# Kernel tuning notes

Measured on AMD Instinct MI355X. Metric: run time of the kernel, lower is better.

Reference implementation:

```python
import jax, jax.numpy as jnp
import numpy as np

H = 256          # LSTM hidden size
P = 1            # proj_size
L = 5            # num LSTM layers
T = 1000         # sequence length (forced by Linear(1000, 100))


def _uniform(key, shape, scale):
    return jax.random.uniform(key, shape, dtype=jnp.float32, minval=-scale, maxval=scale)


def setup_inputs() -> dict:
    key = jax.random.key(0)
    ks = jax.random.split(key, 16)
    B = 128
    s = 1.0 / np.sqrt(H)  # PyTorch LSTM init scale
    inp = {
        "x": jax.random.normal(ks[0], (B, T, 1), dtype=jnp.float32),
        # stacked LSTM params: layer input dim is 1 for all layers (input_size=1, proj_size=1)
        "Wih": _uniform(ks[1], (L, 4 * H, 1), s),
        "Whh": _uniform(ks[2], (L, 4 * H, P), s),
        "bih": _uniform(ks[3], (L, 4 * H), s),
        "bhh": _uniform(ks[4], (L, 4 * H), s),
        "Whr": _uniform(ks[5], (L, P, H), s),
        # MLP head
        "W1": _uniform(ks[6], (100, 1000), 1.0 / np.sqrt(1000)),
        "b1": _uniform(ks[7], (100,), 1.0 / np.sqrt(1000)),
        "W2": _uniform(ks[8], (100, 100), 0.1),
        "b2": _uniform(ks[9], (100,), 0.1),
        "W3": _uniform(ks[10], (100, 100), 0.1),
        "b3": _uniform(ks[11], (100,), 0.1),
        "W4": _uniform(ks[12], (1, 100), 0.1),
        "b4": _uniform(ks[13], (1,), 0.1),
    }
    return inp


def _lstm_layer(x_seq, Wih, Whh, bih, bhh, Whr):
    """One projected LSTM layer. x_seq: [B, T, in_dim] -> [B, T, P]."""
    B = x_seq.shape[0]
    # precompute input contribution for all timesteps: [B, T, 4H]
    gx = jnp.einsum('bti,gi->btg', x_seq, Wih) + bih + bhh
    gx = jnp.transpose(gx, (1, 0, 2))  # [T, B, 4H] for scan

    def step(carry, g_t):
        h, c = carry                      # h: [B, P], c: [B, H]
        gates = g_t + h @ Whh.T           # [B, 4H]
        i = jax.nn.sigmoid(gates[:, 0 * H:1 * H])
        f = jax.nn.sigmoid(gates[:, 1 * H:2 * H])
        g = jnp.tanh(gates[:, 2 * H:3 * H])
        o = jax.nn.sigmoid(gates[:, 3 * H:4 * H])
        c = f * c + i * g
        h = (o * jnp.tanh(c)) @ Whr.T     # projected hidden: [B, P]
        return (h, c), h

    h0 = jnp.zeros((B, P), x_seq.dtype)
    c0 = jnp.zeros((B, H), x_seq.dtype)
    _, hs = jax.lax.scan(step, (h0, c0), gx)  # hs: [T, B, P]
    return jnp.transpose(hs, (1, 0, 2))       # [B, T, P]


def reference(x, Wih, Whh, bih, bhh, Whr, W1, b1, W2, b2, W3, b3, W4, b4):
    out = x
    for l in range(L):  # fixed 5 stacked layers
        out = _lstm_layer(out, Wih[l], Whh[l], bih[l], bhh[l], Whr[l])
    out = out[:, :, 0]                      # squeeze -> [B, 1000]
    out = jax.nn.sigmoid(out @ W1.T + b1)   # linear1 + Sigmoid
    out = jax.nn.sigmoid(out @ W2.T + b2)   # linear2 + Sigmoid
    out = jax.nn.relu(out @ W3.T + b3)      # linear3 + ReLU
    out = out @ W4.T + b4                   # linear4 -> [B, 1]
    return out
```

## Files before the change

### kernel.cpp

```cpp
#include <hip/hip_runtime.h>


#define LAYERS 5
#define TT 1000
#define BATCH 128
#define CH 40
#define NCH (TT / CH)

#define LOG2E 1.4426950408889634f

__device__ __forceinline__ float fast_exp2(float x) {
#if __has_builtin(__builtin_amdgcn_exp2f)
  return __builtin_amdgcn_exp2f(x);
#else
  return __exp2f(x);
#endif
}
__device__ __forceinline__ float fast_rcp(float x) {
#if __has_builtin(__builtin_amdgcn_rcpf)
  return __builtin_amdgcn_rcpf(x);
#else
  return 1.0f / x;
#endif
}
__device__ __forceinline__ float fast_sigmoid(float z) {
  float e = fast_exp2(-LOG2E * z);
  return fast_rcp(1.0f + e);
}

template <int CTRL>
__device__ __forceinline__ float dpp_add(float v) {
  int moved = __builtin_amdgcn_update_dpp(0, __builtin_bit_cast(int, v),
                                          CTRL, 0xF, 0xF, false);
  return v + __builtin_bit_cast(float, moved);
}

__device__ __forceinline__ float wave_sum_uniform(float v) {
  v = dpp_add<0x128>(v);
  v = dpp_add<0x124>(v);
  v = dpp_add<0x122>(v);
  v = dpp_add<0x121>(v);
  v = dpp_add<0x142>(v);
  v = dpp_add<0x143>(v);
  return __builtin_bit_cast(float, __builtin_amdgcn_readlane(__builtin_bit_cast(int, v), 63));
}

__device__ __forceinline__ float lane_bcast(float v, int s) {
  return __builtin_bit_cast(float, __builtin_amdgcn_readlane(__builtin_bit_cast(int, v), s));
}

__global__ __launch_bounds__(64, 1) void lstm_wave_kernel(
    const float* __restrict__ x,
    const float* __restrict__ Wih,
    const float* __restrict__ Whh,
    const float* __restrict__ bih,
    const float* __restrict__ bhh,
    const float* __restrict__ Whr,
    float* __restrict__ seq,
    int* __restrict__ flags)
{
  const int bid  = blockIdx.x;
  const int l    = bid >> 7;
  const int b    = bid & 127;
  const int lane = threadIdx.x;

  float wix[4][4], whx[4][4], gb[4][4], whr[4], cc[4];
  const int base = l * 1024;
#pragma unroll
  for (int g = 0; g < 4; ++g) {
    const float sc = (g == 2) ? (-2.0f * LOG2E) : (-LOG2E);
#pragma unroll
    for (int k = 0; k < 4; ++k) {
      int j = base + g * 256 + k * 64 + lane;
      wix[g][k] = Wih[j] * sc;
      whx[g][k] = Whh[j] * sc;
      gb[g][k]  = (bih[j] + bhh[j]) * sc;
    }
  }
#pragma unroll
  for (int k = 0; k < 4; ++k) {
    whr[k] = Whr[l * 256 + k * 64 + lane];
    cc[k] = 0.0f;
  }

  const float* in  = (l == 0) ? (x + b * TT) : (seq + ((l - 1) * BATCH + b) * TT);
  float*       out = seq + (l * BATCH + b) * TT;
  int*       my_flag = flags + l * BATCH + b;
  const int* in_flag = (l > 0) ? (flags + (l - 1) * BATCH + b) : (const int*)flags;

  float h = 0.0f;
  for (int c = 0; c < NCH; ++c) {
    if (l > 0) {
      while (__hip_atomic_load(in_flag, __ATOMIC_ACQUIRE,
                               __HIP_MEMORY_SCOPE_AGENT) <= c)
        __builtin_amdgcn_s_sleep(2);
    }
    float xv = 0.0f;
    if (lane < CH) {
      if (l == 0)
        xv = in[c * CH + lane];
      else
        xv = __hip_atomic_load(in + c * CH + lane, __ATOMIC_RELAXED,
                               __HIP_MEMORY_SCOPE_AGENT);
    }

    float outv = 0.0f;
#pragma unroll 2
    for (int s = 0; s < CH; ++s) {
      const float xs = lane_bcast(xv, s);

      float gx[4][4];
#pragma unroll
      for (int g = 0; g < 4; ++g)
#pragma unroll
        for (int k = 0; k < 4; ++k)
          gx[g][k] = fmaf(xs, wix[g][k], gb[g][k]);

      float E[4][4];
#pragma unroll
      for (int g = 0; g < 4; ++g)
#pragma unroll
        for (int k = 0; k < 4; ++k)
          E[g][k] = fast_exp2(fmaf(h, whx[g][k], gx[g][k]));

      float rr[4];
#pragma unroll
      for (int k = 0; k < 4; ++k) {
        float ig = fast_rcp(1.0f + E[0][k]);
        float fg = fast_rcp(1.0f + E[1][k]);
        float gg = fmaf(2.0f, fast_rcp(1.0f + E[2][k]), -1.0f);
        float og = fast_rcp(1.0f + E[3][k]);
        cc[k] = fmaf(fg, cc[k], ig * gg);
        float tE = fast_exp2(cc[k] * (-2.0f * LOG2E));
        float tc = fmaf(2.0f, fast_rcp(1.0f + tE), -1.0f);
        rr[k] = og * tc * whr[k];
      }
      float r = (rr[0] + rr[1]) + (rr[2] + rr[3]);

      h = wave_sum_uniform(r);
      if (lane == s) outv = h;
    }

    if (l < 4) {
      if (lane < CH)
        __hip_atomic_store(out + c * CH + lane, outv, __ATOMIC_RELAXED,
                           __HIP_MEMORY_SCOPE_AGENT);
      if (lane == 0)
        __hip_atomic_store(my_flag, c + 1, __ATOMIC_RELEASE,
                           __HIP_MEMORY_SCOPE_AGENT);
    } else {
      if (lane < CH) out[c * CH + lane] = outv;
    }
  }
}

__global__ __launch_bounds__(512) void mlp_head_kernel(
    const float* __restrict__ seq4,
    const float* __restrict__ W1, const float* __restrict__ b1,
    const float* __restrict__ W2, const float* __restrict__ b2,
    const float* __restrict__ W3, const float* __restrict__ b3,
    const float* __restrict__ W4, const float* __restrict__ b4,
    float* __restrict__ out)
{
  __shared__ float sx[TT];
  __shared__ float sh[100];
  __shared__ float sh2[100];
  __shared__ float part[3][100];
  __shared__ float red[8];

  const int b = blockIdx.x, tid = threadIdx.x;
  for (int i = tid; i < TT; i += 512) sx[i] = seq4[b * TT + i];
  __syncthreads();

  const int quarter = tid >> 7;
  const int oid     = tid & 127;
  float myacc = 0.0f;
  if (oid < 100) {
    const float* w  = W1 + oid * TT + quarter * 250;
    const float* xx = sx + quarter * 250;
    float a0 = 0.f, a1 = 0.f;
    for (int t0 = 0; t0 < 250; t0 += 2) {
      float2 v = *(const float2*)(w + t0);
      a0 = fmaf(v.x, xx[t0 + 0], a0);
      a1 = fmaf(v.y, xx[t0 + 1], a1);
    }
    myacc = a0 + a1;
    if (quarter > 0) part[quarter - 1][oid] = myacc;
  }
  __syncthreads();
  if (tid < 100)
    sh[tid] = fast_sigmoid(myacc + part[0][tid] + part[1][tid] + part[2][tid] + b1[tid]);
  __syncthreads();

  if (tid < 100) {
    float acc = b2[tid];
    const float* w = W2 + tid * 100;
    for (int k = 0; k < 100; ++k) acc += w[k] * sh[k];
    sh2[tid] = fast_sigmoid(acc);
  }
  __syncthreads();

  if (tid < 100) {
    float acc = b3[tid];
    const float* w = W3 + tid * 100;
    for (int k = 0; k < 100; ++k) acc += w[k] * sh2[k];
    sh[tid] = fmaxf(acc, 0.0f);
  }
  __syncthreads();

  float r = (tid < 100) ? sh[tid] * W4[tid] : 0.0f;
  r = wave_sum_uniform(r);
  if ((tid & 63) == 0) red[tid >> 6] = r;
  __syncthreads();
  if (tid == 0)
    out[b] = ((red[0] + red[1]) + (red[2] + red[3])) +
             ((red[4] + red[5]) + (red[6] + red[7])) + b4[0];
}

extern "C" void kernel_launch(void* const* d_in, const int* in_sizes, int n_in,
                              void* d_out, int out_size, void* d_ws, size_t ws_size,
                              hipStream_t stream) {
  const float* x   = (const float*)d_in[0];
  const float* Wih = (const float*)d_in[1];
  const float* Whh = (const float*)d_in[2];
  const float* bih = (const float*)d_in[3];
  const float* bhh = (const float*)d_in[4];
  const float* Whr = (const float*)d_in[5];
  const float* W1  = (const float*)d_in[6];
  const float* b1  = (const float*)d_in[7];
  const float* W2  = (const float*)d_in[8];
  const float* b2  = (const float*)d_in[9];
  const float* W3  = (const float*)d_in[10];
  const float* b3  = (const float*)d_in[11];
  const float* W4  = (const float*)d_in[12];
  const float* b4  = (const float*)d_in[13];

  float* seq   = (float*)d_ws;
  int*   flags = (int*)(seq + LAYERS * BATCH * TT);

  hipMemsetAsync(flags, 0, LAYERS * BATCH * sizeof(int), stream);
  lstm_wave_kernel<<<LAYERS * BATCH, 64, 0, stream>>>(x, Wih, Whh, bih, bhh, Whr,
                                                      seq, flags);
  mlp_head_kernel<<<BATCH, 512, 0, stream>>>(seq + 4 * BATCH * TT,
                                             W1, b1, W2, b2, W3, b3, W4, b4,
                                             (float*)d_out);
}
```

Measured before the change: 563.6 us.

## Split LSTM hidden units across two waves and fuse MLP head into pipeline

Each LSTM block now runs two waves, each owning half of the 256 hidden units, and combines the partial projected-h sums through LDS with a block barrier every timestep. This halves the per-wave transcendental work on the serial recurrence. In exchange, every step pays a __syncthreads plus an LDS round-trip. The MLP head moves into extra blocks of the same kernel that consume layer-4 outputs chunk by chunk through flags, so the W1 matvec overlaps the recurrence. This relies on all 768 blocks being co-resident to avoid deadlock.

```diff
diff --git a/kernel.cpp b/kernel.cpp
--- a/kernel.cpp
+++ b/kernel.cpp
@@ -35,186 +35,178 @@
   return v + __builtin_bit_cast(float, moved);
 }
 
-__device__ __forceinline__ float wave_sum_uniform(float v) {
+__device__ __forceinline__ float wave_sum_to_hi(float v) {
   v = dpp_add<0x128>(v);
   v = dpp_add<0x124>(v);
   v = dpp_add<0x122>(v);
   v = dpp_add<0x121>(v);
   v = dpp_add<0x142>(v);
   v = dpp_add<0x143>(v);
-  return __builtin_bit_cast(float, __builtin_amdgcn_readlane(__builtin_bit_cast(int, v), 63));
+  return v;
 }
 
 __device__ __forceinline__ float lane_bcast(float v, int s) {
   return __builtin_bit_cast(float, __builtin_amdgcn_readlane(__builtin_bit_cast(int, v), s));
 }
 
-__global__ __launch_bounds__(64, 1) void lstm_wave_kernel(
+__global__ __launch_bounds__(128) void fused_pipeline_kernel(
     const float* __restrict__ x,
     const float* __restrict__ Wih,
     const float* __restrict__ Whh,
     const float* __restrict__ bih,
     const float* __restrict__ bhh,
     const float* __restrict__ Whr,
-    float* __restrict__ seq,
-    int* __restrict__ flags)
-{
-  const int bid  = blockIdx.x;
-  const int l    = bid >> 7;
-  const int b    = bid & 127;
-  const int lane = threadIdx.x;
-
-  float wix[4][4], whx[4][4], gb[4][4], whr[4], cc[4];
-  const int base = l * 1024;
-#pragma unroll
-  for (int g = 0; g < 4; ++g) {
-    const float sc = (g == 2) ? (-2.0f * LOG2E) : (-LOG2E);
-#pragma unroll
-    for (int k = 0; k < 4; ++k) {
-      int j = base + g * 256 + k * 64 + lane;
-      wix[g][k] = Wih[j] * sc;
-      whx[g][k] = Whh[j] * sc;
-      gb[g][k]  = (bih[j] + bhh[j]) * sc;
-    }
-  }
-#pragma unroll
-  for (int k = 0; k < 4; ++k) {
-    whr[k] = Whr[l * 256 + k * 64 + lane];
-    cc[k] = 0.0f;
-  }
-
-  const float* in  = (l == 0) ? (x + b * TT) : (seq + ((l - 1) * BATCH + b) * TT);
-  float*       out = seq + (l * BATCH + b) * TT;
-  int*       my_flag = flags + l * BATCH + b;
-  const int* in_flag = (l > 0) ? (flags + (l - 1) * BATCH + b) : (const int*)flags;
-
-  float h = 0.0f;
-  for (int c = 0; c < NCH; ++c) {
-    if (l > 0) {
-      while (__hip_atomic_load(in_flag, __ATOMIC_ACQUIRE,
-                               __HIP_MEMORY_SCOPE_AGENT) <= c)
-        __builtin_amdgcn_s_sleep(2);
-    }
-    float xv = 0.0f;
-    if (lane < CH) {
-      if (l == 0)
-        xv = in[c * CH + lane];
-      else
-        xv = __hip_atomic_load(in + c * CH + lane, __ATOMIC_RELAXED,
-                               __HIP_MEMORY_SCOPE_AGENT);
-    }
-
-    float outv = 0.0f;
-#pragma unroll 2
-    for (int s = 0; s < CH; ++s) {
-      const float xs = lane_bcast(xv, s);
-
-      float gx[4][4];
-#pragma unroll
-      for (int g = 0; g < 4; ++g)
-#pragma unroll
-        for (int k = 0; k < 4; ++k)
-          gx[g][k] = fmaf(xs, wix[g][k], gb[g][k]);
-
-      float E[4][4];
-#pragma unroll
-      for (int g = 0; g < 4; ++g)
-#pragma unroll
-        for (int k = 0; k < 4; ++k)
-          E[g][k] = fast_exp2(fmaf(h, whx[g][k], gx[g][k]));
-
-      float rr[4];
-#pragma unroll
-      for (int k = 0; k < 4; ++k) {
-        float ig = fast_rcp(1.0f + E[0][k]);
-        float fg = fast_rcp(1.0f + E[1][k]);
-        float gg = fmaf(2.0f, fast_rcp(1.0f + E[2][k]), -1.0f);
-        float og = fast_rcp(1.0f + E[3][k]);
-        cc[k] = fmaf(fg, cc[k], ig * gg);
-        float tE = fast_exp2(cc[k] * (-2.0f * LOG2E));
-        float tc = fmaf(2.0f, fast_rcp(1.0f + tE), -1.0f);
-        rr[k] = og * tc * whr[k];
-      }
-      float r = (rr[0] + rr[1]) + (rr[2] + rr[3]);
-
-      h = wave_sum_uniform(r);
-      if (lane == s) outv = h;
-    }
-
-    if (l < 4) {
-      if (lane < CH)
-        __hip_atomic_store(out + c * CH + lane, outv, __ATOMIC_RELAXED,
-                           __HIP_MEMORY_SCOPE_AGENT);
-      if (lane == 0)
-        __hip_atomic_store(my_flag, c + 1, __ATOMIC_RELEASE,
-                           __HIP_MEMORY_SCOPE_AGENT);
-    } else {
-      if (lane < CH) out[c * CH + lane] = outv;
-    }
-  }
-}
-
-__global__ __launch_bounds__(512) void mlp_head_kernel(
-    const float* __restrict__ seq4,
     const float* __restrict__ W1, const float* __restrict__ b1,
     const float* __restrict__ W2, const float* __restrict__ b2,
     const float* __restrict__ W3, const float* __restrict__ b3,
     const float* __restrict__ W4, const float* __restrict__ b4,
+    float* __restrict__ seq,
+    int* __restrict__ flags,
     float* __restrict__ out)
 {
-  __shared__ float sx[TT];
+  __shared__ float hx[2][2];
+  __shared__ float shx[CH];
   __shared__ float sh[100];
   __shared__ float sh2[100];
-  __shared__ float part[3][100];
-  __shared__ float red[8];
-
-  const int b = blockIdx.x, tid = threadIdx.x;
-  for (int i = tid; i < TT; i += 512) sx[i] = seq4[b * TT + i];
-  __syncthreads();
-
-  const int quarter = tid >> 7;
-  const int oid     = tid & 127;
-  float myacc = 0.0f;
-  if (oid < 100) {
-    const float* w  = W1 + oid * TT + quarter * 250;
-    const float* xx = sx + quarter * 250;
-    float a0 = 0.f, a1 = 0.f;
-    for (int t0 = 0; t0 < 250; t0 += 2) {
-      float2 v = *(const float2*)(w + t0);
-      a0 = fmaf(v.x, xx[t0 + 0], a0);
-      a1 = fmaf(v.y, xx[t0 + 1], a1);
-    }
-    myacc = a0 + a1;
-    if (quarter > 0) part[quarter - 1][oid] = myacc;
+  __shared__ float red[2];
+
+  const int bid  = blockIdx.x;
+  const int tid  = threadIdx.x;
+  const int w    = tid >> 6;
+  const int lane = tid & 63;
+
+  if (bid < LAYERS * BATCH) {
+    const int l = bid >> 7;
+    const int b = bid & 127;
+
+    float wix[4][2], whx[4][2], gb[4][2], whr[2], cc[2];
+    const int base = l * 1024;
+#pragma unroll
+    for (int g = 0; g < 4; ++g) {
+      const float sc = (g == 2) ? (-2.0f * LOG2E) : (-LOG2E);
+#pragma unroll
+      for (int k2 = 0; k2 < 2; ++k2) {
+        int j = base + g * 256 + (2 * w + k2) * 64 + lane;
+        wix[g][k2] = Wih[j] * sc;
+        whx[g][k2] = Whh[j] * sc;
+        gb[g][k2]  = (bih[j] + bhh[j]) * sc;
+      }
+    }
+#pragma unroll
+    for (int k2 = 0; k2 < 2; ++k2) {
+      whr[k2] = Whr[l * 256 + (2 * w + k2) * 64 + lane];
+      cc[k2] = 0.0f;
+    }
+
+    const float* in  = (l == 0) ? (x + b * TT) : (seq + ((l - 1) * BATCH + b) * TT);
+    float*       outp = seq + (l * BATCH + b) * TT;
+    int*       my_flag = flags + l * BATCH + b;
+    const int* in_flag = flags + (l - 1) * BATCH + b;
+
+    float h = 0.0f;
+    for (int c = 0; c < NCH; ++c) {
+      if (l > 0) {
+        while (__hip_atomic_load(in_flag, __ATOMIC_ACQUIRE,
+                                 __HIP_MEMORY_SCOPE_AGENT) <= c)
+          __builtin_amdgcn_s_sleep(2);
+      }
+      float xv = 0.0f;
+      if (lane < CH) {
+        if (l == 0)
+          xv = in[c * CH + lane];
+        else
+          xv = __hip_atomic_load(in + c * CH + lane, __ATOMIC_RELAXED,
+                                 __HIP_MEMORY_SCOPE_AGENT);
+      }
+
+      float outv = 0.0f;
+      for (int s = 0; s < CH; ++s) {
+        const float xs = lane_bcast(xv, s);
+        float r = 0.0f;
+#pragma unroll
+        for (int k2 = 0; k2 < 2; ++k2) {
+          float e0 = fast_exp2(fmaf(h, whx[0][k2], fmaf(xs, wix[0][k2], gb[0][k2])));
+          float e1 = fast_exp2(fmaf(h, whx[1][k2], fmaf(xs, wix[1][k2], gb[1][k2])));
+          float e2 = fast_exp2(fmaf(h, whx[2][k2], fmaf(xs, wix[2][k2], gb[2][k2])));
+          float e3 = fast_exp2(fmaf(h, whx[3][k2], fmaf(xs, wix[3][k2], gb[3][k2])));
+          float ig = fast_rcp(1.0f + e0);
+          float fg = fast_rcp(1.0f + e1);
+          float gg = fmaf(2.0f, fast_rcp(1.0f + e2), -1.0f);
+          float og = fast_rcp(1.0f + e3);
+          cc[k2] = fmaf(fg, cc[k2], ig * gg);
+          float tE = fast_exp2(cc[k2] * (-2.0f * LOG2E));
+          float tc = fmaf(2.0f, fast_rcp(1.0f + tE), -1.0f);
+          r = fmaf(og * tc, whr[k2], r);
+        }
+        r = wave_sum_to_hi(r);
+        if (lane == 63) hx[s & 1][w] = r;
+        __syncthreads();
+        h = hx[s & 1][0] + hx[s & 1][1];
+        if (w == 0 && lane == s) outv = h;
+      }
+
+      if (w == 0) {
+        if (lane < CH)
+          __hip_atomic_store(outp + c * CH + lane, outv, __ATOMIC_RELAXED,
+                             __HIP_MEMORY_SCOPE_AGENT);
+        if (lane == 0)
+          __hip_atomic_store(my_flag, c + 1, __ATOMIC_RELEASE,
+                             __HIP_MEMORY_SCOPE_AGENT);
+      }
+    }
+  } else {
+    const int b = bid - LAYERS * BATCH;
+    const float* h4 = seq + (4 * BATCH + b) * TT;
+    const int* f4 = flags + 4 * BATCH + b;
+
+    float acc = 0.0f;
+    for (int c = 0; c < NCH; ++c) {
+      while (__hip_atomic_load(f4, __ATOMIC_ACQUIRE,
+                               __HIP_MEMORY_SCOPE_AGENT) <= c)
+        __builtin_amdgcn_s_sleep(16);
+      if (tid < CH)
+        shx[tid] = __hip_atomic_load(h4 + c * CH + tid, __ATOMIC_RELAXED,
+                                     __HIP_MEMORY_SCOPE_AGENT);
+      __syncthreads();
+      if (tid < 100) {
+        const float* wr = W1 + tid * TT + c * CH;
+#pragma unroll
+        for (int j = 0; j < CH; j += 4) {
+          float4 v = *(const float4*)(wr + j);
+          acc = fmaf(v.x, shx[j + 0], acc);
+          acc = fmaf(v.y, shx[j + 1], acc);
+          acc = fmaf(v.z, shx[j + 2], acc);
+          acc = fmaf(v.w, shx[j + 3], acc);
+        }
+      }
+      __syncthreads();
+    }
+
+    if (tid < 100) sh[tid] = fast_sigmoid(acc + b1[tid]);
+    __syncthreads();
+
+    if (tid < 100) {
+      float a = b2[tid];
+      const float* wr = W2 + tid * 100;
+      for (int k = 0; k < 100; ++k) a += wr[k] * sh[k];
+      sh2[tid] = fast_sigmoid(a);
+    }
+    __syncthreads();
+
+    if (tid < 100) {
+      float a = b3[tid];
+      const float* wr = W3 + tid * 100;
+      for (int k = 0; k < 100; ++k) a += wr[k] * sh2[k];
+      sh[tid] = fmaxf(a, 0.0f);
+    }
+    __syncthreads();
+
+    float r = (tid < 100) ? sh[tid] * W4[tid] : 0.0f;
+    r = wave_sum_to_hi(r);
+    if (lane == 63) red[w] = r;
+    __syncthreads();
+    if (tid == 0) out[b] = red[0] + red[1] + b4[0];
   }
-  __syncthreads();
-  if (tid < 100)
-    sh[tid] = fast_sigmoid(myacc + part[0][tid] + part[1][tid] + part[2][tid] + b1[tid]);
-  __syncthreads();
-
-  if (tid < 100) {
-    float acc = b2[tid];
-    const float* w = W2 + tid * 100;
-    for (int k = 0; k < 100; ++k) acc += w[k] * sh[k];
-    sh2[tid] = fast_sigmoid(acc);
-  }
-  __syncthreads();
-
-  if (tid < 100) {
-    float acc = b3[tid];
-    const float* w = W3 + tid * 100;
-    for (int k = 0; k < 100; ++k) acc += w[k] * sh2[k];
-    sh[tid] = fmaxf(acc, 0.0f);
-  }
-  __syncthreads();
-
-  float r = (tid < 100) ? sh[tid] * W4[tid] : 0.0f;
-  r = wave_sum_uniform(r);
-  if ((tid & 63) == 0) red[tid >> 6] = r;
-  __syncthreads();
-  if (tid == 0)
-    out[b] = ((red[0] + red[1]) + (red[2] + red[3])) +
-             ((red[4] + red[5]) + (red[6] + red[7])) + b4[0];
 }
 
 extern "C" void kernel_launch(void* const* d_in, const int* in_sizes, int n_in,
@@ -239,9 +231,7 @@
   int*   flags = (int*)(seq + LAYERS * BATCH * TT);
 
   hipMemsetAsync(flags, 0, LAYERS * BATCH * sizeof(int), stream);
-  lstm_wave_kernel<<<LAYERS * BATCH, 64, 0, stream>>>(x, Wih, Whh, bih, bhh, Whr,
-                                                      seq, flags);
-  mlp_head_kernel<<<BATCH, 512, 0, stream>>>(seq + 4 * BATCH * TT,
-                                             W1, b1, W2, b2, W3, b3, W4, b4,
-                                             (float*)d_out);
-}
+  fused_pipeline_kernel<<<LAYERS * BATCH + BATCH, 128, 0, stream>>>(
+      x, Wih, Whh, bih, bhh, Whr, W1, b1, W2, b2, W3, b3, W4, b4,
+      seq, flags, (float*)d_out);
+}
```

After: 913.5 us. 62.1% more time.

## Fuse MLP head into LSTM pipeline kernel and reduce reciprocals per step

Applied to the files above, without the earlier changes.

Adds 128 extra blocks to the LSTM wavefront kernel. They consume layer-4 outputs chunk by chunk through the flag protocol and accumulate linear1 as the data arrives, which removes the separate MLP launch and its tail. The per-step gate math now shares one reciprocal between each pair of sigmoids (rcp of a product), so fewer transcendental ops sit on the recurrence critical path. The gate input FMAs are also hoisted ahead of the wave reduction, with sched barriers, to overlap independent work. Risks: the extra spinning blocks compete for CUs, and the shared-reciprocal trick can overflow when the exponentials are large.

```diff
diff --git a/kernel.cpp b/kernel.cpp
--- a/kernel.cpp
+++ b/kernel.cpp
@@ -26,6 +26,11 @@
 __device__ __forceinline__ float fast_sigmoid(float z) {
   float e = fast_exp2(-LOG2E * z);
   return fast_rcp(1.0f + e);
+}
+__device__ __forceinline__ void sched_fence() {
+#if __has_builtin(__builtin_amdgcn_sched_barrier)
+  __builtin_amdgcn_sched_barrier(0);
+#endif
 }
 
 template <int CTRL>
@@ -49,172 +54,213 @@
   return __builtin_bit_cast(float, __builtin_amdgcn_readlane(__builtin_bit_cast(int, v), s));
 }
 
-__global__ __launch_bounds__(64, 1) void lstm_wave_kernel(
+__global__ __launch_bounds__(64, 1) void fused_pipeline_kernel(
     const float* __restrict__ x,
     const float* __restrict__ Wih,
     const float* __restrict__ Whh,
     const float* __restrict__ bih,
     const float* __restrict__ bhh,
     const float* __restrict__ Whr,
+    const float* __restrict__ W1, const float* __restrict__ b1,
+    const float* __restrict__ W2, const float* __restrict__ b2,
+    const float* __restrict__ W3, const float* __restrict__ b3,
+    const float* __restrict__ W4, const float* __restrict__ b4,
     float* __restrict__ seq,
-    int* __restrict__ flags)
+    int* __restrict__ flags,
+    float* __restrict__ out)
 {
   const int bid  = blockIdx.x;
-  const int l    = bid >> 7;
-  const int b    = bid & 127;
-  const int lane = threadIdx.x;
-
-  float wix[4][4], whx[4][4], gb[4][4], whr[4], cc[4];
-  const int base = l * 1024;
-#pragma unroll
-  for (int g = 0; g < 4; ++g) {
-    const float sc = (g == 2) ? (-2.0f * LOG2E) : (-LOG2E);
+  const int lane = threadIdx.x & 63;
+
+  if (bid < LAYERS * BATCH) {
+    const int l = bid >> 7;
+    const int b = bid & 127;
+
+    float wix[4][4], whx[4][4], gb[4][4], whr[4], cc[4];
+    const int base = l * 1024;
+#pragma unroll
+    for (int g = 0; g < 4; ++g) {
+      const float sc = (g == 2) ? (-2.0f * LOG2E) : (-LOG2E);
+#pragma unroll
+      for (int k = 0; k < 4; ++k) {
+        int j = base + g * 256 + k * 64 + lane;
+        wix[g][k] = Wih[j] * sc;
+        whx[g][k] = Whh[j] * sc;
+        gb[g][k]  = (bih[j] + bhh[j]) * sc;
+      }
+    }
 #pragma unroll
     for (int k = 0; k < 4; ++k) {
-      int j = base + g * 256 + k * 64 + lane;
-      wix[g][k] = Wih[j] * sc;
-      whx[g][k] = Whh[j] * sc;
-      gb[g][k]  = (bih[j] + bhh[j]) * sc;
-    }
-  }
-#pragma unroll
-  for (int k = 0; k < 4; ++k) {
-    whr[k] = Whr[l * 256 + k * 64 + lane];
-    cc[k] = 0.0f;
-  }
-
-  const float* in  = (l == 0) ? (x + b * TT) : (seq + ((l - 1) * BATCH + b) * TT);
-  float*       out = seq + (l * BATCH + b) * TT;
-  int*       my_flag = flags + l * BATCH + b;
-  const int* in_flag = (l > 0) ? (flags + (l - 1) * BATCH + b) : (const int*)flags;
-
-  float h = 0.0f;
-  for (int c = 0; c < NCH; ++c) {
-    if (l > 0) {
-      while (__hip_atomic_load(in_flag, __ATOMIC_ACQUIRE,
-                               __HIP_MEMORY_SCOPE_AGENT) <= c)
-        __builtin_amdgcn_s_sleep(2);
-    }
-    float xv = 0.0f;
-    if (lane < CH) {
-      if (l == 0)
-        xv = in[c * CH + lane];
-      else
-        xv = __hip_atomic_load(in + c * CH + lane, __ATOMIC_RELAXED,
-                               __HIP_MEMORY_SCOPE_AGENT);
-    }
-
-    float outv = 0.0f;
-#pragma unroll 2
-    for (int s = 0; s < CH; ++s) {
-      const float xs = lane_bcast(xv, s);
-
-      float gx[4][4];
-#pragma unroll
-      for (int g = 0; g < 4; ++g)
-#pragma unroll
-        for (int k = 0; k < 4; ++k)
-          gx[g][k] = fmaf(xs, wix[g][k], gb[g][k]);
-
-      float E[4][4];
-#pragma unroll
-      for (int g = 0; g < 4; ++g)
-#pragma unroll
-        for (int k = 0; k < 4; ++k)
-          E[g][k] = fast_exp2(fmaf(h, whx[g][k], gx[g][k]));
-
-      float rr[4];
+      whr[k] = Whr[l * 256 + k * 64 + lane];
+      cc[k] = 0.0f;
+    }
+
+    auto combine = [&](const float (&E)[4][4]) -> float {
+      float r = 0.0f;
 #pragma unroll
       for (int k = 0; k < 4; ++k) {
-        float ig = fast_rcp(1.0f + E[0][k]);
-        float fg = fast_rcp(1.0f + E[1][k]);
-        float gg = fmaf(2.0f, fast_rcp(1.0f + E[2][k]), -1.0f);
-        float og = fast_rcp(1.0f + E[3][k]);
+        float a0 = 1.0f + E[0][k];
+        float a1 = 1.0f + E[1][k];
+        float a2 = 1.0f + E[2][k];
+        float a3 = 1.0f + E[3][k];
+        float q01 = fast_rcp(a0 * a1);
+        float q23 = fast_rcp(a2 * a3);
+        float ig = q01 * a1;
+        float fg = q01 * a0;
+        float og = q23 * a2;
+        float gg = (1.0f - E[2][k]) * (q23 * a3);
         cc[k] = fmaf(fg, cc[k], ig * gg);
-        float tE = fast_exp2(cc[k] * (-2.0f * LOG2E));
-        float tc = fmaf(2.0f, fast_rcp(1.0f + tE), -1.0f);
-        rr[k] = og * tc * whr[k];
-      }
-      float r = (rr[0] + rr[1]) + (rr[2] + rr[3]);
-
-      h = wave_sum_uniform(r);
-      if (lane == s) outv = h;
-    }
-
-    if (l < 4) {
+        float e4 = fast_exp2(cc[k] * (-2.0f * LOG2E));
+        float q4 = fast_rcp(1.0f + e4);
+        float tc = fmaf(2.0f, q4, -1.0f);
+        r = fmaf(og * tc, whr[k], r);
+      }
+      return r;
+    };
+
+    const float* in  = (l == 0) ? (x + b * TT) : (seq + ((l - 1) * BATCH + b) * TT);
+    float*      outp = seq + (l * BATCH + b) * TT;
+    int*      my_flag = flags + l * BATCH + b;
+    const int* in_flag = flags + (l - 1) * BATCH + b;
+
+    float h = 0.0f;
+    for (int c = 0; c < NCH; ++c) {
+      if (l > 0) {
+        while (__hip_atomic_load(in_flag, __ATOMIC_ACQUIRE,
+                                 __HIP_MEMORY_SCOPE_AGENT) <= c)
+          __builtin_amdgcn_s_sleep(2);
+      }
+      float xv = 0.0f;
+      if (lane < CH) {
+        if (l == 0)
+          xv = in[c * CH + lane];
+        else
+          xv = __hip_atomic_load(in + c * CH + lane, __ATOMIC_RELAXED,
+                                 __HIP_MEMORY_SCOPE_AGENT);
+      }
+
+      float outv = 0.0f;
+      float r_carry;
+      {
+        const float xs = lane_bcast(xv, 0);
+        float E[4][4];
+#pragma unroll
+        for (int g = 0; g < 4; ++g)
+#pragma unroll
+          for (int k = 0; k < 4; ++k)
+            E[g][k] = fast_exp2(fmaf(h, whx[g][k], fmaf(xs, wix[g][k], gb[g][k])));
+        sched_fence();
+        r_carry = combine(E);
+      }
+#pragma unroll 1
+      for (int s = 1; s < CH; ++s) {
+        const float xs = lane_bcast(xv, s);
+        float gx[4][4];
+#pragma unroll
+        for (int g = 0; g < 4; ++g)
+#pragma unroll
+          for (int k = 0; k < 4; ++k)
+            gx[g][k] = fmaf(xs, wix[g][k], gb[g][k]);
+        h = wave_sum_uniform(r_carry);
+        if (lane == s - 1) outv = h;
+        float E[4][4];
+#pragma unroll
+        for (int g = 0; g < 4; ++g)
+#pragma unroll
+          for (int k = 0; k < 4; ++k)
+            E[g][k] = fast_exp2(fmaf(h, whx[g][k], gx[g][k]));
+        sched_fence();
+        r_carry = combine(E);
+      }
+      h = wave_sum_uniform(r_carry);
+      if (lane == CH - 1) outv = h;
+
       if (lane < CH)
-        __hip_atomic_store(out + c * CH + lane, outv, __ATOMIC_RELAXED,
+        __hip_atomic_store(outp + c * CH + lane, outv, __ATOMIC_RELAXED,
                            __HIP_MEMORY_SCOPE_AGENT);
       if (lane == 0)
         __hip_atomic_store(my_flag, c + 1, __ATOMIC_RELEASE,
                            __HIP_MEMORY_SCOPE_AGENT);
-    } else {
-      if (lane < CH) out[c * CH + lane] = outv;
-    }
+    }
+  } else {
+    __shared__ float hbuf[100];
+    __shared__ float hbuf2[100];
+
+    const int b = bid - LAYERS * BATCH;
+    const float* h4 = seq + (4 * BATCH + b) * TT;
+    const int* f4 = flags + 4 * BATCH + b;
+    const int o0 = lane;
+    const int o1 = 64 + lane;
+    const bool has1 = (o1 < 100);
+
+    float acc0 = 0.0f, acc1 = 0.0f;
+    for (int c = 0; c < NCH; ++c) {
+      while (__hip_atomic_load(f4, __ATOMIC_ACQUIRE,
+                               __HIP_MEMORY_SCOPE_AGENT) <= c)
+        __builtin_amdgcn_s_sleep(8);
+      float xv = 0.0f;
+      if (lane < CH)
+        xv = __hip_atomic_load(h4 + c * CH + lane, __ATOMIC_RELAXED,
+                               __HIP_MEMORY_SCOPE_AGENT);
+      const float* w0 = W1 + o0 * TT + c * CH;
+      const float* w1 = W1 + o1 * TT + c * CH;
+#pragma unroll
+      for (int j = 0; j < CH; j += 4) {
+        float4 v0 = *(const float4*)(w0 + j);
+        float x0 = lane_bcast(xv, j + 0);
+        float x1 = lane_bcast(xv, j + 1);
+        float x2 = lane_bcast(xv, j + 2);
+        float x3 = lane_bcast(xv, j + 3);
+        acc0 = fmaf(v0.x, x0, acc0);
+        acc0 = fmaf(v0.y, x1, acc0);
+        acc0 = fmaf(v0.z, x2, acc0);
+        acc0 = fmaf(v0.w, x3, acc0);
+        if (has1) {
+          float4 v1 = *(const float4*)(w1 + j);
+          acc1 = fmaf(v1.x, x0, acc1);
+          acc1 = fmaf(v1.y, x1, acc1);
+          acc1 = fmaf(v1.z, x2, acc1);
+          acc1 = fmaf(v1.w, x3, acc1);
+        }
+      }
+    }
+
+    hbuf[o0] = fast_sigmoid(acc0 + b1[o0]);
+    if (has1) hbuf[o1] = fast_sigmoid(acc1 + b1[o1]);
+    __syncthreads();
+
+    {
+      float a0 = b2[o0], a1 = has1 ? b2[o1] : 0.0f;
+      const float* w0r = W2 + o0 * 100;
+      const float* w1r = W2 + o1 * 100;
+      for (int k = 0; k < 100; ++k) {
+        float hv = hbuf[k];
+        a0 = fmaf(w0r[k], hv, a0);
+        if (has1) a1 = fmaf(w1r[k], hv, a1);
+      }
+      hbuf2[o0] = fast_sigmoid(a0);
+      if (has1) hbuf2[o1] = fast_sigmoid(a1);
+    }
+    __syncthreads();
+
+    {
+      float a0 = b3[o0], a1 = has1 ? b3[o1] : 0.0f;
+      const float* w0r = W3 + o0 * 100;
+      const float* w1r = W3 + o1 * 100;
+      for (int k = 0; k < 100; ++k) {
+        float hv = hbuf2[k];
+        a0 = fmaf(w0r[k], hv, a0);
+        if (has1) a1 = fmaf(w1r[k], hv, a1);
+      }
+      hbuf[o0] = fmaxf(a0, 0.0f);
+      if (has1) hbuf[o1] = fmaxf(a1, 0.0f);
+    }
+    __syncthreads();
+
+    float r = hbuf[o0] * W4[o0] + (has1 ? hbuf[o1] * W4[o1] : 0.0f);
+    r = wave_sum_uniform(r);
+    if (lane == 0) out[b] = r + b4[0];
   }
-}
-
-__global__ __launch_bounds__(512) void mlp_head_kernel(
-    const float* __restrict__ seq4,
-    const float* __restrict__ W1, const float* __restrict__ b1,
-    const float* __restrict__ W2, const float* __restrict__ b2,
-    const float* __restrict__ W3, const float* __restrict__ b3,
-    const float* __restrict__ W4, const float* __restrict__ b4,
-    float* __restrict__ out)
-{
-  __shared__ float sx[TT];
-  __shared__ float sh[100];
-  __shared__ float sh2[100];
-  __shared__ float part[3][100];
-  __shared__ float red[8];
-
-  const int b = blockIdx.x, tid = threadIdx.x;
-  for (int i = tid; i < TT; i += 512) sx[i] = seq4[b * TT + i];
-  __syncthreads();
-
-  const int quarter = tid >> 7;
-  const int oid     = tid & 127;
-  float myacc = 0.0f;
-  if (oid < 100) {
-    const float* w  = W1 + oid * TT + quarter * 250;
-    const float* xx = sx + quarter * 250;
-    float a0 = 0.f, a1 = 0.f;
-    for (int t0 = 0; t0 < 250; t0 += 2) {
-      float2 v = *(const float2*)(w + t0);
-      a0 = fmaf(v.x, xx[t0 + 0], a0);
-      a1 = fmaf(v.y, xx[t0 + 1], a1);
-    }
-    myacc = a0 + a1;
-    if (quarter > 0) part[quarter - 1][oid] = myacc;
-  }
-  __syncthreads();
-  if (tid < 100)
-    sh[tid] = fast_sigmoid(myacc + part[0][tid] + part[1][tid] + part[2][tid] + b1[tid]);
-  __syncthreads();
-
-  if (tid < 100) {
-    float acc = b2[tid];
-    const float* w = W2 + tid * 100;
-    for (int k = 0; k < 100; ++k) acc += w[k] * sh[k];
-    sh2[tid] = fast_sigmoid(acc);
-  }
-  __syncthreads();
-
-  if (tid < 100) {
-    float acc = b3[tid];
-    const float* w = W3 + tid * 100;
-    for (int k = 0; k < 100; ++k) acc += w[k] * sh2[k];
-    sh[tid] = fmaxf(acc, 0.0f);
-  }
-  __syncthreads();
-
-  float r = (tid < 100) ? sh[tid] * W4[tid] : 0.0f;
-  r = wave_sum_uniform(r);
-  if ((tid & 63) == 0) red[tid >> 6] = r;
-  __syncthreads();
-  if (tid == 0)
-    out[b] = ((red[0] + red[1]) + (red[2] + red[3])) +
-             ((red[4] + red[5]) + (red[6] + red[7])) + b4[0];
 }
 
 extern "C" void kernel_launch(void* const* d_in, const int* in_sizes, int n_in,
@@ -239,9 +285,7 @@
   int*   flags = (int*)(seq + LAYERS * BATCH * TT);
 
   hipMemsetAsync(flags, 0, LAYERS * BATCH * sizeof(int), stream);
-  lstm_wave_kernel<<<LAYERS * BATCH, 64, 0, stream>>>(x, Wih, Whh, bih, bhh, Whr,
-                                                      seq, flags);
-  mlp_head_kernel<<<BATCH, 512, 0, stream>>>(seq + 4 * BATCH * TT,
-                                             W1, b1, W2, b2, W3, b3, W4, b4,
-                                             (float*)d_out);
-}
+  fused_pipeline_kernel<<<LAYERS * BATCH + BATCH, 64, 0, stream>>>(
+      x, Wih, Whh, bih, bhh, Whr, W1, b1, W2, b2, W3, b3, W4, b4,
+      seq, flags, (float*)d_out);
+}
```

After: 735.0 us. +30.4%, slower.
